# Optimization experiments

Measured on AMD Instinct MI355X. Metric: run time of the kernel, lower is better.

Reference implementation:

```python
import jax, jax.numpy as jnp
import numpy as np

N_NODES = 100000
N_EDGES = 1600000
N_GRAPHS = 512


def gcn_conv(x, W, b, src, dst, n_nodes):
    """GCNConv with self-loops: D^-1/2 (A+I) D^-1/2 X W + b."""
    h = x @ W  # [N, out]
    ones = jnp.ones((src.shape[0],), h.dtype)
    deg = jax.ops.segment_sum(ones, dst, num_segments=n_nodes) + 1.0  # +1 self-loop
    dinv = jax.lax.rsqrt(deg)
    norm = dinv[src] * dinv[dst]  # [E]
    agg = jax.ops.segment_sum(h[src] * norm[:, None], dst, num_segments=n_nodes)
    agg = agg + h * (1.0 / deg)[:, None]  # self-loop term: deg^-0.5 * deg^-0.5
    return agg + b


def setup_inputs() -> dict:
    key = jax.random.key(0)
    ks = jax.random.split(key, 12)
    x = jax.random.normal(ks[0], (N_NODES, 78), dtype=jnp.float32)
    edge_index = jax.random.randint(ks[1], (2, N_EDGES), 0, N_NODES, dtype=jnp.int64)
    batch = jnp.sort(jax.random.randint(ks[2], (N_NODES,), 0, N_GRAPHS, dtype=jnp.int64))
    def glorot(k, shape):
        lim = np.sqrt(6.0 / (shape[0] + shape[1])).astype(np.float32)
        return jax.random.uniform(k, shape, jnp.float32, -lim, lim)
    return {
        "x": x,
        "edge_index": edge_index,
        "batch": batch,
        "W1": glorot(ks[3], (78, 128)),
        "b1": jnp.zeros((128,), jnp.float32),
        "W2": glorot(ks[4], (128, 256)),
        "b2": jnp.zeros((256,), jnp.float32),
        "Wg1": glorot(ks[5], (256, 1024)),
        "bg1": jnp.zeros((1024,), jnp.float32),
        "Wg2": glorot(ks[6], (1024, 128)),
        "bg2": jnp.zeros((128,), jnp.float32),
    }


def reference(x, edge_index, batch, W1, b1, W2, b2, Wg1, bg1, Wg2, bg2):
    src, dst = edge_index[0], edge_index[1]
    n = x.shape[0]
    h = jax.nn.relu(gcn_conv(x, W1, b1, src, dst, n))   # [N,128]
    h = jax.nn.relu(gcn_conv(h, W2, b2, src, dst, n))   # [N,256]
    g = jax.ops.segment_max(h, batch, num_segments=N_GRAPHS)  # global max pool [G,256]
    g = jax.nn.relu(g @ Wg1 + bg1)   # [G,1024]; dropout is identity at eval
    g = g @ Wg2 + bg2                # [G,128]
    return g
```

## Files before the change

### kernel.cpp

```cpp
#include <hip/hip_runtime.h>
#include <hip/hip_bf16.h>


#define NN 100000
#define NE 1600000
#define NG 512
#define NBLK ((NN + 1023) / 1024)


__global__ void k_zero_int(int* p, int n) {
    int i = blockIdx.x * blockDim.x + threadIdx.x;
    if (i < n) p[i] = 0;
}

__global__ void k_hist(const int* __restrict__ dst, int* cnt, int e) {
    int i = blockIdx.x * blockDim.x + threadIdx.x;
    if (i < e) atomicAdd(&cnt[dst[i]], 1);
}

__global__ void k_prep(const int* __restrict__ cnt, float* __restrict__ dinv,
                       float* __restrict__ gmax) {
    int i = blockIdx.x * blockDim.x + threadIdx.x;
    if (i < NN) dinv[i] = rsqrtf((float)cnt[i] + 1.0f);
    if (i < NG * 256) gmax[i] = 0.0f;
}

__global__ __launch_bounds__(256) void k_bsum(const int* __restrict__ cnt, int* __restrict__ bsum) {
    __shared__ int s[256];
    int b = blockIdx.x, t = threadIdx.x;
    int base = b * 1024 + t * 4;
    int v = 0;
#pragma unroll
    for (int j = 0; j < 4; j++) { int i = base + j; if (i < NN) v += cnt[i]; }
    s[t] = v; __syncthreads();
    for (int off = 128; off > 0; off >>= 1) {
        if (t < off) s[t] += s[t + off];
        __syncthreads();
    }
    if (t == 0) bsum[b] = s[0];
}

__global__ __launch_bounds__(128) void k_scan_bsum(int* bsum, int* row_ptr) {
    __shared__ int s[128];
    int t = threadIdx.x;
    int v = (t < NBLK) ? bsum[t] : 0;
    s[t] = v; __syncthreads();
    for (int off = 1; off < 128; off <<= 1) {
        int u = (t >= off) ? s[t - off] : 0;
        __syncthreads();
        s[t] += u;
        __syncthreads();
    }
    if (t < NBLK) bsum[t] = s[t] - v;
    if (t == 0) row_ptr[NN] = NE;
}

__global__ __launch_bounds__(256) void k_scan_blocks(const int* __restrict__ cnt,
    const int* __restrict__ bsum, int* __restrict__ row_ptr, int* __restrict__ cursor) {
    __shared__ int s[256];
    int b = blockIdx.x, t = threadIdx.x;
    int base = b * 1024 + t * 4;
    int v[4]; int sum = 0;
#pragma unroll
    for (int j = 0; j < 4; j++) { int i = base + j; v[j] = (i < NN) ? cnt[i] : 0; sum += v[j]; }
    s[t] = sum; __syncthreads();
    for (int off = 1; off < 256; off <<= 1) {
        int u = (t >= off) ? s[t - off] : 0;
        __syncthreads();
        s[t] += u;
        __syncthreads();
    }
    int excl = s[t] - sum + bsum[b];
#pragma unroll
    for (int j = 0; j < 4; j++) {
        int i = base + j;
        if (i < NN) { row_ptr[i] = excl; cursor[i] = excl; excl += v[j]; }
    }
}

__global__ void k_fillslots(const int* __restrict__ src, const int* __restrict__ dst,
    const float* __restrict__ dinv, int* cursor, int2* __restrict__ es, int e) {
    int i = blockIdx.x * blockDim.x + threadIdx.x;
    if (i >= e) return;
    int s = src[i], d = dst[i];
    int pos = atomicAdd(&cursor[d], 1);
    es[pos] = make_int2(s, __float_as_int(dinv[s] * dinv[d]));
}

__global__ __launch_bounds__(256) void k_fused1(const float* __restrict__ x,
    const int* __restrict__ rp, const int2* __restrict__ es,
    const float* __restrict__ dinv, const float* __restrict__ W,
    const float* __restrict__ bias, float* __restrict__ out) {
    __shared__ float As[4][8][80];
    int tid = threadIdx.x;
    int wv = tid >> 6, l = tid & 63;
    int task = __builtin_amdgcn_readfirstlane(blockIdx.x * 4 + wv);
    int n0 = task * 8;

    for (int i = 0; i < 8; i++) {
        if (l < 39) {
            int n = n0 + i;
            float di = dinv[n], sw = di * di;
            float2 a = ((const float2*)(x + (size_t)n * 78))[l];
            a.x *= sw; a.y *= sw;
            int e = rp[n], e1 = rp[n + 1];
            int nf = (e1 - e) >> 3;
            if (nf > 0) {
                int2 cur[8];
#pragma unroll
                for (int j = 0; j < 8; j++) cur[j] = es[e + j];
                for (int b = 1; ; b++) {
                    float2 v[8];
#pragma unroll
                    for (int j = 0; j < 8; j++)
                        v[j] = ((const float2*)(x + (size_t)cur[j].x * 78))[l];
                    e += 8;
                    bool more = (b < nf);
                    int2 nxt[8];
                    if (more) {
#pragma unroll
                        for (int j = 0; j < 8; j++) nxt[j] = es[e + j];
                    }
#pragma unroll
                    for (int j = 0; j < 8; j++) {
                        float w = __int_as_float(cur[j].y);
                        a.x += v[j].x * w; a.y += v[j].y * w;
                    }
                    if (!more) break;
#pragma unroll
                    for (int j = 0; j < 8; j++) cur[j] = nxt[j];
                }
            }
            for (; e < e1; e++) {
                int2 p = es[e];
                float w = __int_as_float(p.y);
                float2 v = ((const float2*)(x + (size_t)p.x * 78))[l];
                a.x += v.x * w; a.y += v.y * w;
            }
            *(float2*)&As[wv][i][2 * l] = a;
        }
    }

    int f0 = l * 2;
    float2 acc[8];
#pragma unroll
    for (int i = 0; i < 8; i++) acc[i] = make_float2(0.f, 0.f);

    for (int k = 0; k < 76; k += 4) {
        float2 w0 = *(const float2*)&W[(k + 0) * 128 + f0];
        float2 w1 = *(const float2*)&W[(k + 1) * 128 + f0];
        float2 w2 = *(const float2*)&W[(k + 2) * 128 + f0];
        float2 w3 = *(const float2*)&W[(k + 3) * 128 + f0];
#pragma unroll
        for (int i = 0; i < 8; i++) {
            float4 a = *(const float4*)&As[wv][i][k];
            acc[i].x += a.x * w0.x + a.y * w1.x + a.z * w2.x + a.w * w3.x;
            acc[i].y += a.x * w0.y + a.y * w1.y + a.z * w2.y + a.w * w3.y;
        }
    }
    {
        float2 w0 = *(const float2*)&W[76 * 128 + f0];
        float2 w1 = *(const float2*)&W[77 * 128 + f0];
#pragma unroll
        for (int i = 0; i < 8; i++) {
            float2 a = *(const float2*)&As[wv][i][76];
            acc[i].x += a.x * w0.x + a.y * w1.x;
            acc[i].y += a.x * w0.y + a.y * w1.y;
        }
    }
    float2 bv = *(const float2*)&bias[f0];
#pragma unroll
    for (int i = 0; i < 8; i++) {
        float2 o;
        o.x = fmaxf(acc[i].x + bv.x, 0.f);
        o.y = fmaxf(acc[i].y + bv.y, 0.f);
        *(float2*)&out[(size_t)(n0 + i) * 128 + f0] = o;
    }
}

__global__ __launch_bounds__(256) void k_fused2(const float* __restrict__ h,
    const int* __restrict__ rp, const int2* __restrict__ es,
    const float* __restrict__ dinv, const float* __restrict__ W,
    const float* __restrict__ bias, const int* __restrict__ batch,
    unsigned* __restrict__ gmax) {
    __shared__ float As[4][8][128];
    int tid = threadIdx.x;
    int wv = tid >> 6, l = tid & 63;
    int task = __builtin_amdgcn_readfirstlane(blockIdx.x * 4 + wv);
    int n0 = task * 8;

    for (int i = 0; i < 8; i++) {
        int n = n0 + i;
        float di = dinv[n], sw = di * di;
        float2 a = ((const float2*)(h + (size_t)n * 128))[l];
        a.x *= sw; a.y *= sw;
        int e = rp[n], e1 = rp[n + 1];
        int nf = (e1 - e) >> 3;
        if (nf > 0) {
            int2 cur[8];
#pragma unroll
            for (int j = 0; j < 8; j++) cur[j] = es[e + j];
            for (int b = 1; ; b++) {
                float2 v[8];
#pragma unroll
                for (int j = 0; j < 8; j++)
                    v[j] = ((const float2*)(h + (size_t)cur[j].x * 128))[l];
                e += 8;
                bool more = (b < nf);
                int2 nxt[8];
                if (more) {
#pragma unroll
                    for (int j = 0; j < 8; j++) nxt[j] = es[e + j];
                }
#pragma unroll
                for (int j = 0; j < 8; j++) {
                    float w = __int_as_float(cur[j].y);
                    a.x += v[j].x * w; a.y += v[j].y * w;
                }
                if (!more) break;
#pragma unroll
                for (int j = 0; j < 8; j++) cur[j] = nxt[j];
            }
        }
        for (; e < e1; e++) {
            int2 p = es[e];
            float w = __int_as_float(p.y);
            float2 v = ((const float2*)(h + (size_t)p.x * 128))[l];
            a.x += v.x * w; a.y += v.y * w;
        }
        *(float2*)&As[wv][i][2 * l] = a;
    }

    int f0 = l * 4;
    float4 acc[8];
#pragma unroll
    for (int i = 0; i < 8; i++) acc[i] = make_float4(0.f, 0.f, 0.f, 0.f);

    for (int k = 0; k < 128; k += 4) {
        float4 w0 = *(const float4*)&W[(size_t)(k + 0) * 256 + f0];
        float4 w1 = *(const float4*)&W[(size_t)(k + 1) * 256 + f0];
        float4 w2 = *(const float4*)&W[(size_t)(k + 2) * 256 + f0];
        float4 w3 = *(const float4*)&W[(size_t)(k + 3) * 256 + f0];
#pragma unroll
        for (int i = 0; i < 8; i++) {
            float4 a = *(const float4*)&As[wv][i][k];
            acc[i].x += a.x * w0.x + a.y * w1.x + a.z * w2.x + a.w * w3.x;
            acc[i].y += a.x * w0.y + a.y * w1.y + a.z * w2.y + a.w * w3.y;
            acc[i].z += a.x * w0.z + a.y * w1.z + a.z * w2.z + a.w * w3.z;
            acc[i].w += a.x * w0.w + a.y * w1.w + a.z * w2.w + a.w * w3.w;
        }
    }

    float4 bv = *(const float4*)&bias[f0];
    int curg = -1;
    float4 m = make_float4(0.f, 0.f, 0.f, 0.f);
#pragma unroll
    for (int i = 0; i < 8; i++) {
        int g = batch[n0 + i];
        float4 v;
        v.x = fmaxf(acc[i].x + bv.x, 0.f); v.y = fmaxf(acc[i].y + bv.y, 0.f);
        v.z = fmaxf(acc[i].z + bv.z, 0.f); v.w = fmaxf(acc[i].w + bv.w, 0.f);
        if (g != curg) {
            if (curg >= 0) {
                unsigned* gp = &gmax[(size_t)curg * 256 + f0];
                atomicMax(&gp[0], __float_as_uint(m.x));
                atomicMax(&gp[1], __float_as_uint(m.y));
                atomicMax(&gp[2], __float_as_uint(m.z));
                atomicMax(&gp[3], __float_as_uint(m.w));
            }
            curg = g; m = v;
        } else {
            m.x = fmaxf(m.x, v.x); m.y = fmaxf(m.y, v.y);
            m.z = fmaxf(m.z, v.z); m.w = fmaxf(m.w, v.w);
        }
    }
    if (curg >= 0) {
        unsigned* gp = &gmax[(size_t)curg * 256 + f0];
        atomicMax(&gp[0], __float_as_uint(m.x));
        atomicMax(&gp[1], __float_as_uint(m.y));
        atomicMax(&gp[2], __float_as_uint(m.z));
        atomicMax(&gp[3], __float_as_uint(m.w));
    }
}


__global__ __launch_bounds__(256) void k_gemm3(const float* __restrict__ A,
    const float* __restrict__ W, const float* __restrict__ bias,
    float* __restrict__ out) {
    __shared__ float rs[256];
    int g = blockIdx.x, tid = threadIdx.x;
    rs[tid] = A[g * 256 + tid];
    __syncthreads();
    float acc[4] = {0.f, 0.f, 0.f, 0.f};
    for (int k = 0; k < 256; k++) {
        float a = rs[k];
#pragma unroll
        for (int j = 0; j < 4; j++) acc[j] += a * W[k * 1024 + tid + j * 256];
    }
#pragma unroll
    for (int j = 0; j < 4; j++) {
        int f = tid + j * 256;
        out[g * 1024 + f] = fmaxf(acc[j] + bias[f], 0.0f);
    }
}

__global__ __launch_bounds__(128) void k_gemm4(const float* __restrict__ A,
    const float* __restrict__ W, const float* __restrict__ bias,
    float* __restrict__ out) {
    __shared__ float rs[1024];
    int g = blockIdx.x, tid = threadIdx.x;
    for (int i = tid; i < 1024; i += 128) rs[i] = A[g * 1024 + i];
    __syncthreads();
    float acc = 0.0f;
    for (int k = 0; k < 1024; k++) acc += rs[k] * W[k * 128 + tid];
    out[g * 128 + tid] = acc + bias[tid];
}

extern "C" void kernel_launch(void* const* d_in, const int* in_sizes, int n_in,
                              void* d_out, int out_size, void* d_ws, size_t ws_size,
                              hipStream_t stream) {
    const float* x    = (const float*)d_in[0];
    const int*   ei   = (const int*)d_in[1];
    const int*   batch= (const int*)d_in[2];
    const float* W1   = (const float*)d_in[3];
    const float* b1   = (const float*)d_in[4];
    const float* W2   = (const float*)d_in[5];
    const float* b2   = (const float*)d_in[6];
    const float* Wg1  = (const float*)d_in[7];
    const float* bg1  = (const float*)d_in[8];
    const float* Wg2  = (const float*)d_in[9];
    const float* bg2  = (const float*)d_in[10];
    const int* src = ei;
    const int* dst = ei + NE;

    char* w8 = (char*)d_ws;
    int*   cnt     = (int*)w8;                 w8 += (size_t)NN * 4;
    int*   row_ptr = (int*)w8;                 w8 += (size_t)(NN + 4) * 4;
    int*   cursor  = (int*)w8;                 w8 += (size_t)NN * 4;
    int*   bsum    = (int*)w8;                 w8 += 128 * 4;
    int2*  es      = (int2*)w8;                w8 += (size_t)NE * 8;
    float* dinv    = (float*)w8;               w8 += (size_t)NN * 4;
    float* h1      = (float*)w8;               w8 += (size_t)NN * 128 * 4;
    unsigned* gmax = (unsigned*)w8;            w8 += (size_t)NG * 256 * 4;
    float* g1      = (float*)w8;               w8 += (size_t)NG * 1024 * 4;

    k_zero_int<<<(NN + 255) / 256, 256, 0, stream>>>(cnt, NN);
    k_hist<<<(NE + 255) / 256, 256, 0, stream>>>(dst, cnt, NE);
    k_prep<<<(NG * 256 + 255) / 256, 256, 0, stream>>>(cnt, dinv, (float*)gmax);
    k_bsum<<<NBLK, 256, 0, stream>>>(cnt, bsum);
    k_scan_bsum<<<1, 128, 0, stream>>>(bsum, row_ptr);
    k_scan_blocks<<<NBLK, 256, 0, stream>>>(cnt, bsum, row_ptr, cursor);
    k_fillslots<<<(NE + 255) / 256, 256, 0, stream>>>(src, dst, dinv, cursor, es, NE);

    k_fused1<<<NN / 32, 256, 0, stream>>>(x, row_ptr, es, dinv, W1, b1, h1);

    k_fused2<<<NN / 32, 256, 0, stream>>>(h1, row_ptr, es, dinv, W2, b2, batch, gmax);

    k_gemm3<<<NG, 256, 0, stream>>>((const float*)gmax, Wg1, bg1, g1);
    k_gemm4<<<NG, 128, 0, stream>>>(g1, Wg2, bg2, (float*)d_out);
}
```

Measured before the change: 626.6 us.

## Warp-specialize fused GCN kernels into producer gather and consumer GEMM waves

Both fused GCN layer kernels become persistent 512-thread blocks. Six waves gather neighbor features for a 24-node tile into a double-buffered shared array, while two waves run the dense transform on the previous tile, so the latency-bound gather overlaps the compute. In exchange there is a block-wide barrier per tile, fewer waves doing the gather, and possible load imbalance between producer and consumer waves.

Result: slower. 948.0 us (+51.3%).

```diff
diff --git a/kernel.cpp b/kernel.cpp
--- a/kernel.cpp
+++ b/kernel.cpp
@@ -6,6 +6,8 @@
 #define NE 1600000
 #define NG 512
 #define NBLK ((NN + 1023) / 1024)
+#define T2 24
+#define NT ((NN + T2 - 1) / T2)
 
 
 __global__ void k_zero_int(int* p, int n) {
@@ -87,180 +89,229 @@
     es[pos] = make_int2(s, __float_as_int(dinv[s] * dinv[d]));
 }
 
-__global__ __launch_bounds__(256) void k_fused1(const float* __restrict__ x,
+__global__ __launch_bounds__(512) void k_fused1_pc(const float* __restrict__ x,
     const int* __restrict__ rp, const int2* __restrict__ es,
     const float* __restrict__ dinv, const float* __restrict__ W,
     const float* __restrict__ bias, float* __restrict__ out) {
-    __shared__ float As[4][8][80];
+    __shared__ float As[2][T2][80];
     int tid = threadIdx.x;
     int wv = tid >> 6, l = tid & 63;
-    int task = __builtin_amdgcn_readfirstlane(blockIdx.x * 4 + wv);
-    int n0 = task * 8;
-
-    for (int i = 0; i < 8; i++) {
-        if (l < 39) {
-            int n = n0 + i;
-            float di = dinv[n], sw = di * di;
-            float2 a = ((const float2*)(x + (size_t)n * 78))[l];
-            a.x *= sw; a.y *= sw;
-            int e = rp[n], e1 = rp[n + 1];
-            int nf = (e1 - e) >> 3;
-            if (nf > 0) {
-                int2 cur[8];
-#pragma unroll
-                for (int j = 0; j < 8; j++) cur[j] = es[e + j];
-                for (int b = 1; ; b++) {
-                    float2 v[8];
-#pragma unroll
-                    for (int j = 0; j < 8; j++)
-                        v[j] = ((const float2*)(x + (size_t)cur[j].x * 78))[l];
-                    e += 8;
-                    bool more = (b < nf);
-                    int2 nxt[8];
-                    if (more) {
-#pragma unroll
-                        for (int j = 0; j < 8; j++) nxt[j] = es[e + j];
+    int t = blockIdx.x;
+    const int G = gridDim.x;
+    int tprev = -1;
+    int pbuf = 0;
+
+    while (t < NT || tprev >= 0) {
+        if (wv < 6) {
+            if (t < NT && l < 39) {
+#pragma unroll 1
+                for (int i = 0; i < 4; i++) {
+                    int li = wv * 4 + i;
+                    int n = t * T2 + li;
+                    if (n < NN) {
+                        float di = dinv[n], sw = di * di;
+                        float2 a = ((const float2*)(x + (size_t)n * 78))[l];
+                        a.x *= sw; a.y *= sw;
+                        int e = rp[n], e1 = rp[n + 1];
+                        int nf = (e1 - e) >> 3;
+                        if (nf > 0) {
+                            int2 cur[8];
+#pragma unroll
+                            for (int j = 0; j < 8; j++) cur[j] = es[e + j];
+                            for (int b = 1; ; b++) {
+                                float2 v[8];
+#pragma unroll
+                                for (int j = 0; j < 8; j++)
+                                    v[j] = ((const float2*)(x + (size_t)cur[j].x * 78))[l];
+                                e += 8;
+                                bool more = (b < nf);
+                                int2 nxt[8];
+                                if (more) {
+#pragma unroll
+                                    for (int j = 0; j < 8; j++) nxt[j] = es[e + j];
+                                }
+#pragma unroll
+                                for (int j = 0; j < 8; j++) {
+                                    float w = __int_as_float(cur[j].y);
+                                    a.x += v[j].x * w; a.y += v[j].y * w;
+                                }
+                                if (!more) break;
+#pragma unroll
+                                for (int j = 0; j < 8; j++) cur[j] = nxt[j];
+                            }
+                        }
+                        for (; e < e1; e++) {
+                            int2 p = es[e];
+                            float w = __int_as_float(p.y);
+                            float2 v = ((const float2*)(x + (size_t)p.x * 78))[l];
+                            a.x += v.x * w; a.y += v.y * w;
+                        }
+                        *(float2*)&As[pbuf][li][2 * l] = a;
                     }
-#pragma unroll
-                    for (int j = 0; j < 8; j++) {
-                        float w = __int_as_float(cur[j].y);
-                        a.x += v[j].x * w; a.y += v[j].y * w;
-                    }
-                    if (!more) break;
-#pragma unroll
-                    for (int j = 0; j < 8; j++) cur[j] = nxt[j];
-                }
-            }
-            for (; e < e1; e++) {
-                int2 p = es[e];
-                float w = __int_as_float(p.y);
-                float2 v = ((const float2*)(x + (size_t)p.x * 78))[l];
-                a.x += v.x * w; a.y += v.y * w;
-            }
-            *(float2*)&As[wv][i][2 * l] = a;
+                }
+            }
+        } else if (tprev >= 0) {
+            int cw = wv - 6;
+            int rb = pbuf ^ 1;
+            int base = cw * 12;
+            int f0 = l * 2;
+            float2 acc[12];
+#pragma unroll
+            for (int i = 0; i < 12; i++) acc[i] = make_float2(0.f, 0.f);
+
+            for (int k = 0; k < 76; k += 4) {
+                float2 w0 = *(const float2*)&W[(k + 0) * 128 + f0];
+                float2 w1 = *(const float2*)&W[(k + 1) * 128 + f0];
+                float2 w2 = *(const float2*)&W[(k + 2) * 128 + f0];
+                float2 w3 = *(const float2*)&W[(k + 3) * 128 + f0];
+#pragma unroll
+                for (int i = 0; i < 12; i++) {
+                    float4 a = *(const float4*)&As[rb][base + i][k];
+                    acc[i].x += a.x * w0.x + a.y * w1.x + a.z * w2.x + a.w * w3.x;
+                    acc[i].y += a.x * w0.y + a.y * w1.y + a.z * w2.y + a.w * w3.y;
+                }
+            }
+            {
+                float2 w0 = *(const float2*)&W[76 * 128 + f0];
+                float2 w1 = *(const float2*)&W[77 * 128 + f0];
+#pragma unroll
+                for (int i = 0; i < 12; i++) {
+                    float2 a = *(const float2*)&As[rb][base + i][76];
+                    acc[i].x += a.x * w0.x + a.y * w1.x;
+                    acc[i].y += a.x * w0.y + a.y * w1.y;
+                }
+            }
+            float2 bv = *(const float2*)&bias[f0];
+#pragma unroll
+            for (int i = 0; i < 12; i++) {
+                int n = tprev * T2 + base + i;
+                if (n < NN) {
+                    float2 o;
+                    o.x = fmaxf(acc[i].x + bv.x, 0.f);
+                    o.y = fmaxf(acc[i].y + bv.y, 0.f);
+                    *(float2*)&out[(size_t)n * 128 + f0] = o;
+                }
+            }
         }
-    }
-
-    int f0 = l * 2;
-    float2 acc[8];
-#pragma unroll
-    for (int i = 0; i < 8; i++) acc[i] = make_float2(0.f, 0.f);
-
-    for (int k = 0; k < 76; k += 4) {
-        float2 w0 = *(const float2*)&W[(k + 0) * 128 + f0];
-        float2 w1 = *(const float2*)&W[(k + 1) * 128 + f0];
-        float2 w2 = *(const float2*)&W[(k + 2) * 128 + f0];
-        float2 w3 = *(const float2*)&W[(k + 3) * 128 + f0];
-#pragma unroll
-        for (int i = 0; i < 8; i++) {
-            float4 a = *(const float4*)&As[wv][i][k];
-            acc[i].x += a.x * w0.x + a.y * w1.x + a.z * w2.x + a.w * w3.x;
-            acc[i].y += a.x * w0.y + a.y * w1.y + a.z * w2.y + a.w * w3.y;
-        }
-    }
-    {
-        float2 w0 = *(const float2*)&W[76 * 128 + f0];
-        float2 w1 = *(const float2*)&W[77 * 128 + f0];
-#pragma unroll
-        for (int i = 0; i < 8; i++) {
-            float2 a = *(const float2*)&As[wv][i][76];
-            acc[i].x += a.x * w0.x + a.y * w1.x;
-            acc[i].y += a.x * w0.y + a.y * w1.y;
-        }
-    }
-    float2 bv = *(const float2*)&bias[f0];
-#pragma unroll
-    for (int i = 0; i < 8; i++) {
-        float2 o;
-        o.x = fmaxf(acc[i].x + bv.x, 0.f);
-        o.y = fmaxf(acc[i].y + bv.y, 0.f);
-        *(float2*)&out[(size_t)(n0 + i) * 128 + f0] = o;
-    }
-}
-
-__global__ __launch_bounds__(256) void k_fused2(const float* __restrict__ h,
+        __syncthreads();
+        tprev = (t < NT) ? t : -1;
+        t += G;
+        pbuf ^= 1;
+    }
+}
+
+__global__ __launch_bounds__(512) void k_fused2_pc(const float* __restrict__ h,
     const int* __restrict__ rp, const int2* __restrict__ es,
     const float* __restrict__ dinv, const float* __restrict__ W,
     const float* __restrict__ bias, const int* __restrict__ batch,
     unsigned* __restrict__ gmax) {
-    __shared__ float As[4][8][128];
+    __shared__ float As[2][T2][128];
     int tid = threadIdx.x;
     int wv = tid >> 6, l = tid & 63;
-    int task = __builtin_amdgcn_readfirstlane(blockIdx.x * 4 + wv);
-    int n0 = task * 8;
-
-    for (int i = 0; i < 8; i++) {
-        int n = n0 + i;
-        float di = dinv[n], sw = di * di;
-        float2 a = ((const float2*)(h + (size_t)n * 128))[l];
-        a.x *= sw; a.y *= sw;
-        int e = rp[n], e1 = rp[n + 1];
-        int nf = (e1 - e) >> 3;
-        if (nf > 0) {
-            int2 cur[8];
-#pragma unroll
-            for (int j = 0; j < 8; j++) cur[j] = es[e + j];
-            for (int b = 1; ; b++) {
-                float2 v[8];
-#pragma unroll
-                for (int j = 0; j < 8; j++)
-                    v[j] = ((const float2*)(h + (size_t)cur[j].x * 128))[l];
-                e += 8;
-                bool more = (b < nf);
-                int2 nxt[8];
-                if (more) {
-#pragma unroll
-                    for (int j = 0; j < 8; j++) nxt[j] = es[e + j];
-                }
-#pragma unroll
-                for (int j = 0; j < 8; j++) {
-                    float w = __int_as_float(cur[j].y);
-                    a.x += v[j].x * w; a.y += v[j].y * w;
-                }
-                if (!more) break;
-#pragma unroll
-                for (int j = 0; j < 8; j++) cur[j] = nxt[j];
-            }
-        }
-        for (; e < e1; e++) {
-            int2 p = es[e];
-            float w = __int_as_float(p.y);
-            float2 v = ((const float2*)(h + (size_t)p.x * 128))[l];
-            a.x += v.x * w; a.y += v.y * w;
-        }
-        *(float2*)&As[wv][i][2 * l] = a;
-    }
-
-    int f0 = l * 4;
-    float4 acc[8];
-#pragma unroll
-    for (int i = 0; i < 8; i++) acc[i] = make_float4(0.f, 0.f, 0.f, 0.f);
-
-    for (int k = 0; k < 128; k += 4) {
-        float4 w0 = *(const float4*)&W[(size_t)(k + 0) * 256 + f0];
-        float4 w1 = *(const float4*)&W[(size_t)(k + 1) * 256 + f0];
-        float4 w2 = *(const float4*)&W[(size_t)(k + 2) * 256 + f0];
-        float4 w3 = *(const float4*)&W[(size_t)(k + 3) * 256 + f0];
-#pragma unroll
-        for (int i = 0; i < 8; i++) {
-            float4 a = *(const float4*)&As[wv][i][k];
-            acc[i].x += a.x * w0.x + a.y * w1.x + a.z * w2.x + a.w * w3.x;
-            acc[i].y += a.x * w0.y + a.y * w1.y + a.z * w2.y + a.w * w3.y;
-            acc[i].z += a.x * w0.z + a.y * w1.z + a.z * w2.z + a.w * w3.z;
-            acc[i].w += a.x * w0.w + a.y * w1.w + a.z * w2.w + a.w * w3.w;
-        }
-    }
-
-    float4 bv = *(const float4*)&bias[f0];
-    int curg = -1;
-    float4 m = make_float4(0.f, 0.f, 0.f, 0.f);
-#pragma unroll
-    for (int i = 0; i < 8; i++) {
-        int g = batch[n0 + i];
-        float4 v;
-        v.x = fmaxf(acc[i].x + bv.x, 0.f); v.y = fmaxf(acc[i].y + bv.y, 0.f);
-        v.z = fmaxf(acc[i].z + bv.z, 0.f); v.w = fmaxf(acc[i].w + bv.w, 0.f);
-        if (g != curg) {
+    int t = blockIdx.x;
+    const int G = gridDim.x;
+    int tprev = -1;
+    int pbuf = 0;
+
+    while (t < NT || tprev >= 0) {
+        if (wv < 6) {
+            if (t < NT) {
+#pragma unroll 1
+                for (int i = 0; i < 4; i++) {
+                    int li = wv * 4 + i;
+                    int n = t * T2 + li;
+                    if (n < NN) {
+                        float di = dinv[n], sw = di * di;
+                        float2 a = ((const float2*)(h + (size_t)n * 128))[l];
+                        a.x *= sw; a.y *= sw;
+                        int e = rp[n], e1 = rp[n + 1];
+                        int nf = (e1 - e) >> 3;
+                        if (nf > 0) {
+                            int2 cur[8];
+#pragma unroll
+                            for (int j = 0; j < 8; j++) cur[j] = es[e + j];
+                            for (int b = 1; ; b++) {
+                                float2 v[8];
+#pragma unroll
+                                for (int j = 0; j < 8; j++)
+                                    v[j] = ((const float2*)(h + (size_t)cur[j].x * 128))[l];
+                                e += 8;
+                                bool more = (b < nf);
+                                int2 nxt[8];
+                                if (more) {
+#pragma unroll
+                                    for (int j = 0; j < 8; j++) nxt[j] = es[e + j];
+                                }
+#pragma unroll
+                                for (int j = 0; j < 8; j++) {
+                                    float w = __int_as_float(cur[j].y);
+                                    a.x += v[j].x * w; a.y += v[j].y * w;
+                                }
+                                if (!more) break;
+#pragma unroll
+                                for (int j = 0; j < 8; j++) cur[j] = nxt[j];
+                            }
+                        }
+                        for (; e < e1; e++) {
+                            int2 p = es[e];
+                            float w = __int_as_float(p.y);
+                            float2 v = ((const float2*)(h + (size_t)p.x * 128))[l];
+                            a.x += v.x * w; a.y += v.y * w;
+                        }
+                        *(float2*)&As[pbuf][li][2 * l] = a;
+                    }
+                }
+            }
+        } else if (tprev >= 0) {
+            int cw = wv - 6;
+            int rb = pbuf ^ 1;
+            int base = cw * 12;
+            int f0 = l * 4;
+            float4 acc[12];
+#pragma unroll
+            for (int i = 0; i < 12; i++) acc[i] = make_float4(0.f, 0.f, 0.f, 0.f);
+
+            for (int k = 0; k < 128; k += 4) {
+                float4 w0 = *(const float4*)&W[(size_t)(k + 0) * 256 + f0];
+                float4 w1 = *(const float4*)&W[(size_t)(k + 1) * 256 + f0];
+                float4 w2 = *(const float4*)&W[(size_t)(k + 2) * 256 + f0];
+                float4 w3 = *(const float4*)&W[(size_t)(k + 3) * 256 + f0];
+#pragma unroll
+                for (int i = 0; i < 12; i++) {
+                    float4 a = *(const float4*)&As[rb][base + i][k];
+                    acc[i].x += a.x * w0.x + a.y * w1.x + a.z * w2.x + a.w * w3.x;
+                    acc[i].y += a.x * w0.y + a.y * w1.y + a.z * w2.y + a.w * w3.y;
+                    acc[i].z += a.x * w0.z + a.y * w1.z + a.z * w2.z + a.w * w3.z;
+                    acc[i].w += a.x * w0.w + a.y * w1.w + a.z * w2.w + a.w * w3.w;
+                }
+            }
+
+            float4 bv = *(const float4*)&bias[f0];
+            int curg = -1;
+            float4 m = make_float4(0.f, 0.f, 0.f, 0.f);
+#pragma unroll
+            for (int i = 0; i < 12; i++) {
+                int n = tprev * T2 + base + i;
+                if (n < NN) {
+                    int g = batch[n];
+                    float4 v;
+                    v.x = fmaxf(acc[i].x + bv.x, 0.f); v.y = fmaxf(acc[i].y + bv.y, 0.f);
+                    v.z = fmaxf(acc[i].z + bv.z, 0.f); v.w = fmaxf(acc[i].w + bv.w, 0.f);
+                    if (g != curg) {
+                        if (curg >= 0) {
+                            unsigned* gp = &gmax[(size_t)curg * 256 + f0];
+                            atomicMax(&gp[0], __float_as_uint(m.x));
+                            atomicMax(&gp[1], __float_as_uint(m.y));
+                            atomicMax(&gp[2], __float_as_uint(m.z));
+                            atomicMax(&gp[3], __float_as_uint(m.w));
+                        }
+                        curg = g; m = v;
+                    } else {
+                        m.x = fmaxf(m.x, v.x); m.y = fmaxf(m.y, v.y);
+                        m.z = fmaxf(m.z, v.z); m.w = fmaxf(m.w, v.w);
+                    }
+                }
+            }
             if (curg >= 0) {
                 unsigned* gp = &gmax[(size_t)curg * 256 + f0];
                 atomicMax(&gp[0], __float_as_uint(m.x));
@@ -268,18 +319,11 @@
                 atomicMax(&gp[2], __float_as_uint(m.z));
                 atomicMax(&gp[3], __float_as_uint(m.w));
             }
-            curg = g; m = v;
-        } else {
-            m.x = fmaxf(m.x, v.x); m.y = fmaxf(m.y, v.y);
-            m.z = fmaxf(m.z, v.z); m.w = fmaxf(m.w, v.w);
         }
-    }
-    if (curg >= 0) {
-        unsigned* gp = &gmax[(size_t)curg * 256 + f0];
-        atomicMax(&gp[0], __float_as_uint(m.x));
-        atomicMax(&gp[1], __float_as_uint(m.y));
-        atomicMax(&gp[2], __float_as_uint(m.z));
-        atomicMax(&gp[3], __float_as_uint(m.w));
+        __syncthreads();
+        tprev = (t < NT) ? t : -1;
+        t += G;
+        pbuf ^= 1;
     }
 }
 
@@ -352,9 +396,9 @@
     k_scan_blocks<<<NBLK, 256, 0, stream>>>(cnt, bsum, row_ptr, cursor);
     k_fillslots<<<(NE + 255) / 256, 256, 0, stream>>>(src, dst, dinv, cursor, es, NE);
 
-    k_fused1<<<NN / 32, 256, 0, stream>>>(x, row_ptr, es, dinv, W1, b1, h1);
-
-    k_fused2<<<NN / 32, 256, 0, stream>>>(h1, row_ptr, es, dinv, W2, b2, batch, gmax);
+    k_fused1_pc<<<1024, 512, 0, stream>>>(x, row_ptr, es, dinv, W1, b1, h1);
+
+    k_fused2_pc<<<1024, 512, 0, stream>>>(h1, row_ptr, es, dinv, W2, b2, batch, gmax);
 
     k_gemm3<<<NG, 256, 0, stream>>>((const float*)gmax, Wg1, bg1, g1);
     k_gemm4<<<NG, 128, 0, stream>>>(g1, Wg2, bg2, (float*)d_out);
```

## Interleave neighbor gathers for node pairs and use packed FMA in layer-2 GEMM

Applied to the files above, without the earlier changes.

Both fused GCN kernels now aggregate two destination nodes at once, issuing the edge-list loads and feature gathers for both nodes before accumulating. This raises memory-level parallelism and hides gather latency, but drops the previous software prefetch of the next edge chunk. The layer-2 dense transform is rewritten with 2-wide vector FMAs so the compiler can emit packed FP32 FMA instructions. An early return for out-of-range tasks is also added. Together these raise register pressure, which may lower occupancy.

Measured after the change: 587.5 us. 6.2% less time.

```diff
diff --git a/kernel.cpp b/kernel.cpp
--- a/kernel.cpp
+++ b/kernel.cpp
@@ -6,6 +6,8 @@
 #define NE 1600000
 #define NG 512
 #define NBLK ((NN + 1023) / 1024)
+
+typedef float v2f __attribute__((ext_vector_type(2)));
 
 
 __global__ void k_zero_int(int* p, int n) {
@@ -96,48 +98,82 @@
     int wv = tid >> 6, l = tid & 63;
     int task = __builtin_amdgcn_readfirstlane(blockIdx.x * 4 + wv);
     int n0 = task * 8;
-
-    for (int i = 0; i < 8; i++) {
-        if (l < 39) {
-            int n = n0 + i;
-            float di = dinv[n], sw = di * di;
-            float2 a = ((const float2*)(x + (size_t)n * 78))[l];
-            a.x *= sw; a.y *= sw;
-            int e = rp[n], e1 = rp[n + 1];
-            int nf = (e1 - e) >> 3;
-            if (nf > 0) {
-                int2 cur[8];
-#pragma unroll
-                for (int j = 0; j < 8; j++) cur[j] = es[e + j];
-                for (int b = 1; ; b++) {
-                    float2 v[8];
+    if (n0 >= NN) return;
+
+    if (l < 39) {
+        for (int pi = 0; pi < 4; pi++) {
+            int nA = n0 + 2 * pi, nB = nA + 1;
+            float diA = dinv[nA], swA = diA * diA;
+            float diB = dinv[nB], swB = diB * diB;
+            float2 aA = ((const float2*)(x + (size_t)nA * 78))[l];
+            float2 aB = ((const float2*)(x + (size_t)nB * 78))[l];
+            aA.x *= swA; aA.y *= swA;
+            aB.x *= swB; aB.y *= swB;
+            int eA = rp[nA], eA1 = rp[nA + 1];
+            int eB = rp[nB], eB1 = rp[nB + 1];
+            int cA = (eA1 - eA) >> 3, cB = (eB1 - eB) >> 3;
+            while (cA > 0 || cB > 0) {
+                bool dA = (cA > 0), dB = (cB > 0);
+                int2 esA[8], esB[8];
+                float2 vA[8], vB[8];
+                if (dA) {
+#pragma unroll
+                    for (int j = 0; j < 8; j++) esA[j] = es[eA + j];
+                }
+                if (dB) {
+#pragma unroll
+                    for (int j = 0; j < 8; j++) esB[j] = es[eB + j];
+                }
+                if (dA) {
 #pragma unroll
                     for (int j = 0; j < 8; j++)
-                        v[j] = ((const float2*)(x + (size_t)cur[j].x * 78))[l];
-                    e += 8;
-                    bool more = (b < nf);
-                    int2 nxt[8];
-                    if (more) {
-#pragma unroll
-                        for (int j = 0; j < 8; j++) nxt[j] = es[e + j];
+                        vA[j] = ((const float2*)(x + (size_t)esA[j].x * 78))[l];
+                }
+                if (dB) {
+#pragma unroll
+                    for (int j = 0; j < 8; j++)
+                        vB[j] = ((const float2*)(x + (size_t)esB[j].x * 78))[l];
+                }
+                if (dA) {
+#pragma unroll
+                    for (int j = 0; j < 8; j++) {
+                        float w = __int_as_float(esA[j].y);
+                        aA.x += vA[j].x * w; aA.y += vA[j].y * w;
                     }
+                    eA += 8; cA--;
+                }
+                if (dB) {
 #pragma unroll
                     for (int j = 0; j < 8; j++) {
-                        float w = __int_as_float(cur[j].y);
-                        a.x += v[j].x * w; a.y += v[j].y * w;
+                        float w = __int_as_float(esB[j].y);
+                        aB.x += vB[j].x * w; aB.y += vB[j].y * w;
                     }
-                    if (!more) break;
-#pragma unroll
-                    for (int j = 0; j < 8; j++) cur[j] = nxt[j];
-                }
-            }
-            for (; e < e1; e++) {
-                int2 p = es[e];
+                    eB += 8; cB--;
+                }
+            }
+            while (eA < eA1 && eB < eB1) {
+                int2 pA = es[eA], pB = es[eB];
+                float2 vA2 = ((const float2*)(x + (size_t)pA.x * 78))[l];
+                float2 vB2 = ((const float2*)(x + (size_t)pB.x * 78))[l];
+                float wA = __int_as_float(pA.y), wB = __int_as_float(pB.y);
+                aA.x += vA2.x * wA; aA.y += vA2.y * wA;
+                aB.x += vB2.x * wB; aB.y += vB2.y * wB;
+                eA++; eB++;
+            }
+            for (; eA < eA1; eA++) {
+                int2 p = es[eA];
                 float w = __int_as_float(p.y);
                 float2 v = ((const float2*)(x + (size_t)p.x * 78))[l];
-                a.x += v.x * w; a.y += v.y * w;
-            }
-            *(float2*)&As[wv][i][2 * l] = a;
+                aA.x += v.x * w; aA.y += v.y * w;
+            }
+            for (; eB < eB1; eB++) {
+                int2 p = es[eB];
+                float w = __int_as_float(p.y);
+                float2 v = ((const float2*)(x + (size_t)p.x * 78))[l];
+                aB.x += v.x * w; aB.y += v.y * w;
+            }
+            *(float2*)&As[wv][2 * pi][2 * l] = aA;
+            *(float2*)&As[wv][2 * pi + 1][2 * l] = aB;
         }
     }
 
@@ -188,66 +224,109 @@
     int wv = tid >> 6, l = tid & 63;
     int task = __builtin_amdgcn_readfirstlane(blockIdx.x * 4 + wv);
     int n0 = task * 8;
-
-    for (int i = 0; i < 8; i++) {
-        int n = n0 + i;
-        float di = dinv[n], sw = di * di;
-        float2 a = ((const float2*)(h + (size_t)n * 128))[l];
-        a.x *= sw; a.y *= sw;
-        int e = rp[n], e1 = rp[n + 1];
-        int nf = (e1 - e) >> 3;
-        if (nf > 0) {
-            int2 cur[8];
-#pragma unroll
-            for (int j = 0; j < 8; j++) cur[j] = es[e + j];
-            for (int b = 1; ; b++) {
-                float2 v[8];
+    if (n0 >= NN) return;
+
+    for (int pi = 0; pi < 4; pi++) {
+        int nA = n0 + 2 * pi, nB = nA + 1;
+        float diA = dinv[nA], swA = diA * diA;
+        float diB = dinv[nB], swB = diB * diB;
+        float2 aA = ((const float2*)(h + (size_t)nA * 128))[l];
+        float2 aB = ((const float2*)(h + (size_t)nB * 128))[l];
+        aA.x *= swA; aA.y *= swA;
+        aB.x *= swB; aB.y *= swB;
+        int eA = rp[nA], eA1 = rp[nA + 1];
+        int eB = rp[nB], eB1 = rp[nB + 1];
+        int cA = (eA1 - eA) >> 3, cB = (eB1 - eB) >> 3;
+        while (cA > 0 || cB > 0) {
+            bool dA = (cA > 0), dB = (cB > 0);
+            int2 esA[8], esB[8];
+            float2 vA[8], vB[8];
+            if (dA) {
+#pragma unroll
+                for (int j = 0; j < 8; j++) esA[j] = es[eA + j];
+            }
+            if (dB) {
+#pragma unroll
+                for (int j = 0; j < 8; j++) esB[j] = es[eB + j];
+            }
+            if (dA) {
 #pragma unroll
                 for (int j = 0; j < 8; j++)
-                    v[j] = ((const float2*)(h + (size_t)cur[j].x * 128))[l];
-                e += 8;
-                bool more = (b < nf);
-                int2 nxt[8];
-                if (more) {
-#pragma unroll
-                    for (int j = 0; j < 8; j++) nxt[j] = es[e + j];
-                }
+                    vA[j] = ((const float2*)(h + (size_t)esA[j].x * 128))[l];
+            }
+            if (dB) {
+#pragma unroll
+                for (int j = 0; j < 8; j++)
+                    vB[j] = ((const float2*)(h + (size_t)esB[j].x * 128))[l];
+            }
+            if (dA) {
 #pragma unroll
                 for (int j = 0; j < 8; j++) {
-                    float w = __int_as_float(cur[j].y);
-                    a.x += v[j].x * w; a.y += v[j].y * w;
-                }
-                if (!more) break;
-#pragma unroll
-                for (int j = 0; j < 8; j++) cur[j] = nxt[j];
-            }
-        }
-        for (; e < e1; e++) {
-            int2 p = es[e];
+                    float w = __int_as_float(esA[j].y);
+                    aA.x += vA[j].x * w; aA.y += vA[j].y * w;
+                }
+                eA += 8; cA--;
+            }
+            if (dB) {
+#pragma unroll
+                for (int j = 0; j < 8; j++) {
+                    float w = __int_as_float(esB[j].y);
+                    aB.x += vB[j].x * w; aB.y += vB[j].y * w;
+                }
+                eB += 8; cB--;
+            }
+        }
+        while (eA < eA1 && eB < eB1) {
+            int2 pA = es[eA], pB = es[eB];
+            float2 vA2 = ((const float2*)(h + (size_t)pA.x * 128))[l];
+            float2 vB2 = ((const float2*)(h + (size_t)pB.x * 128))[l];
+            float wA = __int_as_float(pA.y), wB = __int_as_float(pB.y);
+            aA.x += vA2.x * wA; aA.y += vA2.y * wA;
+            aB.x += vB2.x * wB; aB.y += vB2.y * wB;
+            eA++; eB++;
+        }
+        for (; eA < eA1; eA++) {
+            int2 p = es[eA];
             float w = __int_as_float(p.y);
             float2 v = ((const float2*)(h + (size_t)p.x * 128))[l];
-            a.x += v.x * w; a.y += v.y * w;
-        }
-        *(float2*)&As[wv][i][2 * l] = a;
+            aA.x += v.x * w; aA.y += v.y * w;
+        }
+        for (; eB < eB1; eB++) {
+            int2 p = es[eB];
+            float w = __int_as_float(p.y);
+            float2 v = ((const float2*)(h + (size_t)p.x * 128))[l];
+            aB.x += v.x * w; aB.y += v.y * w;
+        }
+        *(float2*)&As[wv][2 * pi][2 * l] = aA;
+        *(float2*)&As[wv][2 * pi + 1][2 * l] = aB;
     }
 
     int f0 = l * 4;
-    float4 acc[8];
-#pragma unroll
-    for (int i = 0; i < 8; i++) acc[i] = make_float4(0.f, 0.f, 0.f, 0.f);
+    v2f acc[8][2];
+#pragma unroll
+    for (int i = 0; i < 8; i++) { acc[i][0] = (v2f)(0.f); acc[i][1] = (v2f)(0.f); }
 
     for (int k = 0; k < 128; k += 4) {
         float4 w0 = *(const float4*)&W[(size_t)(k + 0) * 256 + f0];
         float4 w1 = *(const float4*)&W[(size_t)(k + 1) * 256 + f0];
         float4 w2 = *(const float4*)&W[(size_t)(k + 2) * 256 + f0];
         float4 w3 = *(const float4*)&W[(size_t)(k + 3) * 256 + f0];
+        v2f w0a = {w0.x, w0.y}, w0b = {w0.z, w0.w};
+        v2f w1a = {w1.x, w1.y}, w1b = {w1.z, w1.w};
+        v2f w2a = {w2.x, w2.y}, w2b = {w2.z, w2.w};
+        v2f w3a = {w3.x, w3.y}, w3b = {w3.z, w3.w};
 #pragma unroll
         for (int i = 0; i < 8; i++) {
             float4 a = *(const float4*)&As[wv][i][k];
-            acc[i].x += a.x * w0.x + a.y * w1.x + a.z * w2.x + a.w * w3.x;
-            acc[i].y += a.x * w0.y + a.y * w1.y + a.z * w2.y + a.w * w3.y;
-            acc[i].z += a.x * w0.z + a.y * w1.z + a.z * w2.z + a.w * w3.z;
-            acc[i].w += a.x * w0.w + a.y * w1.w + a.z * w2.w + a.w * w3.w;
+            v2f sx = {a.x, a.x}, sy = {a.y, a.y}, sz = {a.z, a.z}, sw = {a.w, a.w};
+            acc[i][0] = __builtin_elementwise_fma(sx, w0a, acc[i][0]);
+            acc[i][1] = __builtin_elementwise_fma(sx, w0b, acc[i][1]);
+            acc[i][0] = __builtin_elementwise_fma(sy, w1a, acc[i][0]);
+            acc[i][1] = __builtin_elementwise_fma(sy, w1b, acc[i][1]);
+            acc[i][0] = __builtin_elementwise_fma(sz, w2a, acc[i][0]);
+            acc[i][1] = __builtin_elementwise_fma(sz, w2b, acc[i][1]);
+            acc[i][0] = __builtin_elementwise_fma(sw, w3a, acc[i][0]);
+            acc[i][1] = __builtin_elementwise_fma(sw, w3b, acc[i][1]);
         }
     }
 
@@ -258,8 +337,8 @@
     for (int i = 0; i < 8; i++) {
         int g = batch[n0 + i];
         float4 v;
-        v.x = fmaxf(acc[i].x + bv.x, 0.f); v.y = fmaxf(acc[i].y + bv.y, 0.f);
-        v.z = fmaxf(acc[i].z + bv.z, 0.f); v.w = fmaxf(acc[i].w + bv.w, 0.f);
+        v.x = fmaxf(acc[i][0].x + bv.x, 0.f); v.y = fmaxf(acc[i][0].y + bv.y, 0.f);
+        v.z = fmaxf(acc[i][1].x + bv.z, 0.f); v.w = fmaxf(acc[i][1].y + bv.w, 0.f);
         if (g != curg) {
             if (curg >= 0) {
                 unsigned* gp = &gmax[(size_t)curg * 256 + f0];
```
